# Optimization experiments

Hardware: AMD Instinct MI355X
Metric: run time of the kernel (lower is better)

## Reference

```python
import jax, jax.numpy as jnp
import numpy as np

HALF = 6.0
MAXC = 63.0
M_EMA = 0.999

def _pooled_ema(feature, pre, fea):
    # feature: [b,c,64,64]; pre: [b,21,2] float coords; fea: [21,c] EMA state
    b, c, H, W = feature.shape
    x = pre[..., 0]
    y = pre[..., 1]
    # torch: clamp then .int() (truncation == floor for non-negative values)
    down = jnp.maximum(y - HALF, 0.0).astype(jnp.int32)   # [b,21]
    left = jnp.maximum(x - HALF, 0.0).astype(jnp.int32)
    upper = jnp.minimum(y + HALF, MAXC).astype(jnp.int32)
    right = jnp.minimum(x + HALF, MAXC).astype(jnp.int32)
    # divisor uses inclusive window size (s1*s2), even though the torch slice
    # feature[:, left:right, down:upper] is exclusive at right/upper (faithful quirk)
    s = ((upper - down + 1) * (right - left + 1)).astype(feature.dtype)  # [b,21]
    # integral image (padded) -> rectangle sum over [left,right) x [down,upper)
    P = jnp.pad(jnp.cumsum(jnp.cumsum(feature, axis=2), axis=3),
                ((0, 0), (0, 0), (1, 0), (1, 0)))  # [b,c,H+1,W+1]
    bi = jnp.arange(b)[:, None]  # [b,1] broadcasts with [b,21] indices
    rect = (P[bi, :, right, upper] - P[bi, :, left, upper]
            - P[bi, :, right, down] + P[bi, :, left, down])  # [b,21,c]
    f4 = rect / s[..., None]          # per-landmark average pool [b,21,c]
    fea_c = f4.mean(axis=0)           # average over batch -> [21,c]
    return M_EMA * fea_c + (1.0 - M_EMA) * fea


def setup_inputs() -> dict:
    key = jax.random.key(0)
    k1, k2, k3, k4 = jax.random.split(key, 4)
    b, c, H, W, L = 64, 256, 64, 64, 21
    f1 = jax.random.uniform(k1, (b, c, H, W), dtype=jnp.float32)
    f2 = jax.random.uniform(k2, (b, c, H, W), dtype=jnp.float32)
    pre1 = jax.random.uniform(k3, (b, L, 2), dtype=jnp.float32) * 63.0
    pre2 = jax.random.uniform(k4, (b, L, 2), dtype=jnp.float32) * 63.0
    fea1 = jnp.zeros((L, c), dtype=jnp.float32)
    fea2 = jnp.zeros((L, c), dtype=jnp.float32)
    return {"f1": f1, "f2": f2, "pre1": pre1, "pre2": pre2,
            "fea1": fea1, "fea2": fea2}


def reference(f1, f2, pre1, pre2, fea1, fea2):
    fea_c1 = _pooled_ema(f1, pre1, fea1)               # [21,c]
    log_p = jax.nn.log_softmax(fea_c1, axis=-1)
    fea_c2 = _pooled_ema(f2, pre2, fea2)               # [21,c]
    q = fea_c2 / fea_c2.sum(axis=-1, keepdims=True)
    # KLDivLoss(reduction='none'): q * (log q - log_p), zero where q == 0
    kl = jnp.where(q > 0, q * (jnp.log(jnp.where(q > 0, q, 1.0)) - log_p), 0.0)
    return kl.sum(axis=-1).mean()
```

## Files before the change

### kernel.cpp

```cpp
#include <hip/hip_runtime.h>

#define NL 21
#define NC 256
#define NB 64

__global__ __launch_bounds__(256) void pool_kernel(const float* __restrict__ feat,
                                                   const float* __restrict__ pre,
                                                   float* __restrict__ acc ) {
    const int blk = blockIdx.x;
    const int b = blk >> 8;
    const int c = blk & 255;

    __shared__ float plane[64 * 68];
    __shared__ float part[256];
    __shared__ int s_left[NL], s_right[NL], s_down[NL], s_upper[NL];
    __shared__ float s_invs[NL];

    const int t = threadIdx.x;

    if (t < NL) {
        const float x = pre[(b * NL + t) * 2 + 0];
        const float y = pre[(b * NL + t) * 2 + 1];
        const int down  = (int)fmaxf(y - 6.0f, 0.0f);
        const int left  = (int)fmaxf(x - 6.0f, 0.0f);
        const int upper = (int)fminf(y + 6.0f, 63.0f);
        const int right = (int)fminf(x + 6.0f, 63.0f);
        s_left[t] = left; s_right[t] = right; s_down[t] = down; s_upper[t] = upper;
        s_invs[t] = 1.0f / (float)((upper - down + 1) * (right - left + 1));
    }

    const float4* __restrict__ src =
        (const float4*)(feat + ((size_t)b * NC + c) * 4096);
#pragma unroll
    for (int k = 0; k < 4; ++k) {
        const int f = t + k * 256;
        const int row = f >> 4;
        const int col4 = f & 15;
        const float4 v = src[f];
        float* dst = &plane[row * 68 + col4 * 4];
        dst[0] = v.x; dst[1] = v.y; dst[2] = v.z; dst[3] = v.w;
    }
    __syncthreads();

    float val = 0.0f;
    if (t < NL * 12) {
        const int l = t / 12;
        const int k = t - l * 12;
        const int h = s_left[l] + k;
        if (h < s_right[l]) {
            const float* row = &plane[h * 68];
            const int d = s_down[l], u = s_upper[l];
            float s = 0.0f;
            for (int w = d; w < u; ++w) s += row[w];
            val = s;
        }
    }
    part[t] = val;
    __syncthreads();

    if (t < NL) {
        float r = 0.0f;
#pragma unroll
        for (int k = 0; k < 12; ++k) r += part[t * 12 + k];
        atomicAdd(&acc[t * NC + c], r * s_invs[t]);
    }
}

__device__ __forceinline__ float wave_sum(float v) {
#pragma unroll
    for (int o = 32; o > 0; o >>= 1) v += __shfl_xor(v, o, 64);
    return v;
}
__device__ __forceinline__ float wave_max(float v) {
#pragma unroll
    for (int o = 32; o > 0; o >>= 1) v = fmaxf(v, __shfl_xor(v, o, 64));
    return v;
}

__device__ __forceinline__ float block_sum(float v, float* red) {
    v = wave_sum(v);
    const int wave = threadIdx.x >> 6, lane = threadIdx.x & 63;
    __syncthreads();
    if (lane == 0) red[wave] = v;
    __syncthreads();
    return red[0] + red[1] + red[2] + red[3];
}
__device__ __forceinline__ float block_max(float v, float* red) {
    v = wave_max(v);
    const int wave = threadIdx.x >> 6, lane = threadIdx.x & 63;
    __syncthreads();
    if (lane == 0) red[wave] = v;
    __syncthreads();
    return fmaxf(fmaxf(red[0], red[1]), fmaxf(red[2], red[3]));
}

__global__ __launch_bounds__(256) void finish_kernel(const float* __restrict__ acc1,
                                                     const float* __restrict__ acc2,
                                                     const float* __restrict__ fea1,
                                                     const float* __restrict__ fea2,
                                                     float* __restrict__ out) {
    const int c = threadIdx.x;
    __shared__ float red[4];

    double total = 0.0;
    for (int l = 0; l < NL; ++l) {
        const int idx = l * NC + c;
        const float x1 = 0.999f * (acc1[idx] * (1.0f / 64.0f)) + 0.001f * fea1[idx];
        const float x2 = 0.999f * (acc2[idx] * (1.0f / 64.0f)) + 0.001f * fea2[idx];

        const float m = block_max(x1, red);
        const float e = __expf(x1 - m);
        const float se = block_sum(e, red);
        const float logZ = m + logf(se);
        const float logp = x1 - logZ;

        const float ssum = block_sum(x2, red);
        const float q = x2 / ssum;

        const float kl = (q > 0.0f) ? q * (logf(q) - logp) : 0.0f;
        const float klrow = block_sum(kl, red);
        total += (double)klrow;
    }
    if (c == 0) out[0] = (float)(total / 21.0);
}

extern "C" void kernel_launch(void* const* d_in, const int* in_sizes, int n_in,
                              void* d_out, int out_size, void* d_ws, size_t ws_size,
                              hipStream_t stream) {
    const float* f1   = (const float*)d_in[0];
    const float* f2   = (const float*)d_in[1];
    const float* pre1 = (const float*)d_in[2];
    const float* pre2 = (const float*)d_in[3];
    const float* fea1 = (const float*)d_in[4];
    const float* fea2 = (const float*)d_in[5];
    float* out = (float*)d_out;

    float* acc1 = (float*)d_ws;
    float* acc2 = acc1 + NL * NC;

    hipMemsetAsync(d_ws, 0, 2 * NL * NC * sizeof(float), stream);

    const dim3 grid(NB * NC), block(256);
    pool_kernel<<<grid, block, 0, stream>>>(f1, pre1, acc1);
    pool_kernel<<<grid, block, 0, stream>>>(f2, pre2, acc2);
    finish_kernel<<<1, 256, 0, stream>>>(acc1, acc2, fea1, fea2, out);
}
```

Baseline: 534.8 us.

## Replace atomics with per-batch partials and merge both pool launches

The pool kernel now writes per-batch partial averages to a workspace buffer instead of issuing atomicAdds into a shared accumulator, which removes the memset and atomic contention. Both feature tensors are handled in one launch through a 2D grid, so one kernel launch goes away. The single-block finish kernel now reduces the 64 batch partials itself and stages the results in shared memory. The cost is a serial reduction over 64×21 loads per thread inside that one block, and about 43 KB of shared memory.

Result: slower. 588.1 us (+10.0%).

```diff
diff --git a/kernel.cpp b/kernel.cpp
--- a/kernel.cpp
+++ b/kernel.cpp
@@ -3,15 +3,20 @@
 #define NL 21
 #define NC 256
 #define NB 64
+#define PSTRIDE 68
 
-__global__ __launch_bounds__(256) void pool_kernel(const float* __restrict__ feat,
-                                                   const float* __restrict__ pre,
-                                                   float* __restrict__ acc ) {
+__global__ __launch_bounds__(256) void pool_kernel(
+    const float* __restrict__ f1, const float* __restrict__ f2,
+    const float* __restrict__ pre1, const float* __restrict__ pre2,
+    float* __restrict__ part1, float* __restrict__ part2) {
     const int blk = blockIdx.x;
     const int b = blk >> 8;
     const int c = blk & 255;
+    const float* __restrict__ feat = blockIdx.y ? f2 : f1;
+    const float* __restrict__ pre  = blockIdx.y ? pre2 : pre1;
+    float* __restrict__ outp       = blockIdx.y ? part2 : part1;
 
-    __shared__ float plane[64 * 68];
+    __shared__ float plane[64 * PSTRIDE];
     __shared__ float part[256];
     __shared__ int s_left[NL], s_right[NL], s_down[NL], s_upper[NL];
     __shared__ float s_invs[NL];
@@ -37,7 +42,7 @@
         const int row = f >> 4;
         const int col4 = f & 15;
         const float4 v = src[f];
-        float* dst = &plane[row * 68 + col4 * 4];
+        float* dst = &plane[row * PSTRIDE + col4 * 4];
         dst[0] = v.x; dst[1] = v.y; dst[2] = v.z; dst[3] = v.w;
     }
     __syncthreads();
@@ -48,7 +53,7 @@
         const int k = t - l * 12;
         const int h = s_left[l] + k;
         if (h < s_right[l]) {
-            const float* row = &plane[h * 68];
+            const float* row = &plane[h * PSTRIDE];
             const int d = s_down[l], u = s_upper[l];
             float s = 0.0f;
             for (int w = d; w < u; ++w) s += row[w];
@@ -62,7 +67,7 @@
         float r = 0.0f;
 #pragma unroll
         for (int k = 0; k < 12; ++k) r += part[t * 12 + k];
-        atomicAdd(&acc[t * NC + c], r * s_invs[t]);
+        outp[((size_t)b * NL + t) * NC + c] = r * s_invs[t];
     }
 }
 
@@ -76,7 +81,6 @@
     for (int o = 32; o > 0; o >>= 1) v = fmaxf(v, __shfl_xor(v, o, 64));
     return v;
 }
-
 __device__ __forceinline__ float block_sum(float v, float* red) {
     v = wave_sum(v);
     const int wave = threadIdx.x >> 6, lane = threadIdx.x & 63;
@@ -94,19 +98,36 @@
     return fmaxf(fmaxf(red[0], red[1]), fmaxf(red[2], red[3]));
 }
 
-__global__ __launch_bounds__(256) void finish_kernel(const float* __restrict__ acc1,
-                                                     const float* __restrict__ acc2,
-                                                     const float* __restrict__ fea1,
-                                                     const float* __restrict__ fea2,
-                                                     float* __restrict__ out) {
+__global__ __launch_bounds__(256) void finish_kernel(
+    const float* __restrict__ part1, const float* __restrict__ part2,
+    const float* __restrict__ fea1, const float* __restrict__ fea2,
+    float* __restrict__ out) {
     const int c = threadIdx.x;
     __shared__ float red[4];
+    __shared__ float sc1[NL][NC];
+    __shared__ float sc2[NL][NC];
+
+    float a1[NL], a2[NL];
+#pragma unroll
+    for (int l = 0; l < NL; ++l) { a1[l] = 0.0f; a2[l] = 0.0f; }
+    for (int b = 0; b < NB; ++b) {
+#pragma unroll
+        for (int l = 0; l < NL; ++l) {
+            a1[l] += part1[((size_t)b * NL + l) * NC + c];
+            a2[l] += part2[((size_t)b * NL + l) * NC + c];
+        }
+    }
+#pragma unroll
+    for (int l = 0; l < NL; ++l) {
+        sc1[l][c] = 0.999f * (a1[l] * (1.0f / 64.0f)) + 0.001f * fea1[l * NC + c];
+        sc2[l][c] = 0.999f * (a2[l] * (1.0f / 64.0f)) + 0.001f * fea2[l * NC + c];
+    }
+    __syncthreads();
 
     double total = 0.0;
     for (int l = 0; l < NL; ++l) {
-        const int idx = l * NC + c;
-        const float x1 = 0.999f * (acc1[idx] * (1.0f / 64.0f)) + 0.001f * fea1[idx];
-        const float x2 = 0.999f * (acc2[idx] * (1.0f / 64.0f)) + 0.001f * fea2[idx];
+        const float x1 = sc1[l][c];
+        const float x2 = sc2[l][c];
 
         const float m = block_max(x1, red);
         const float e = __expf(x1 - m);
@@ -118,8 +139,7 @@
         const float q = x2 / ssum;
 
         const float kl = (q > 0.0f) ? q * (logf(q) - logp) : 0.0f;
-        const float klrow = block_sum(kl, red);
-        total += (double)klrow;
+        total += (double)block_sum(kl, red);
     }
     if (c == 0) out[0] = (float)(total / 21.0);
 }
@@ -135,13 +155,9 @@
     const float* fea2 = (const float*)d_in[5];
     float* out = (float*)d_out;
 
-    float* acc1 = (float*)d_ws;
-    float* acc2 = acc1 + NL * NC;
+    float* part1 = (float*)d_ws;
+    float* part2 = part1 + (size_t)NB * NL * NC;
 
-    hipMemsetAsync(d_ws, 0, 2 * NL * NC * sizeof(float), stream);
-
-    const dim3 grid(NB * NC), block(256);
-    pool_kernel<<<grid, block, 0, stream>>>(f1, pre1, acc1);
-    pool_kernel<<<grid, block, 0, stream>>>(f2, pre2, acc2);
-    finish_kernel<<<1, 256, 0, stream>>>(acc1, acc2, fea1, fea2, out);
+    pool_kernel<<<dim3(NB * NC, 2), 256, 0, stream>>>(f1, f2, pre1, pre2, part1, part2);
+    finish_kernel<<<1, 256, 0, stream>>>(part1, part2, fea1, fea2, out);
 }
```
